# Optimization experiments

Hardware: AMD Instinct MI355X
Metric: run time of the kernel (lower is better)

Reference implementation:

```python
import jax, jax.numpy as jnp
import numpy as np
import math

B, C, BINS, W = 2, 8, 1024, 512
HEADS = 16
HD = BINS // HEADS          # 64 head dim
ROT = BINS // HEADS // 2    # 32 rotated dims
EXP = 4
EPS = 1e-5
MAX_FREQ = 10.0


def setup_inputs() -> dict:
    key = jax.random.key(0)
    ks = jax.random.split(key, 8)
    def u(k, shape, fan_in):
        lim = 1.0 / math.sqrt(fan_in)
        return jax.random.uniform(k, shape, jnp.float32, -lim, lim)
    return {
        "x": jax.random.normal(ks[0], (B, C, BINS, W), jnp.float32),
        "norm1_w": jnp.ones((BINS,), jnp.float32),
        "norm1_b": jnp.zeros((BINS,), jnp.float32),
        # 'pixel' rotary init: linspace(1, max_freq/2, dim//2) * pi (learned)
        "rot_freqs": jnp.linspace(1.0, MAX_FREQ / 2, ROT // 2, dtype=jnp.float32) * math.pi,
        "q_w": u(ks[1], (C, BINS, BINS), BINS),
        "out_w": u(ks[2], (C, BINS, BINS), BINS),
        "norm2_w": jnp.ones((BINS,), jnp.float32),
        "norm2_b": jnp.zeros((BINS,), jnp.float32),
        "lin1_w": u(ks[3], (C, BINS * EXP, BINS), BINS),
        "lin2_w": u(ks[4], (C, BINS, BINS * EXP), BINS * EXP),
    }


def _mlin(x, w):
    # x: [b,c,f_in,w]; w: [c,f_out,f_in] -> [b,c,f_out,w]
    return jnp.einsum('bcfw,cgf->bcgw', x, w)


def _frame_norm(x, w, b):
    # LayerNorm over the bins axis (axis=2) of [b,c,bins,w]
    m = jnp.mean(x, axis=2, keepdims=True)
    v = jnp.var(x, axis=2, keepdims=True)
    xn = (x - m) * jax.lax.rsqrt(v + EPS)
    return xn * w[:, None] + b[:, None]


def _rotate(q, cos, sin):
    # q: [b,c,h,w,d]; rotate first ROT dims with interleaved-pair rotate_half
    q1, q2 = q[..., :ROT], q[..., ROT:]
    qp = q1.reshape(*q1.shape[:-1], ROT // 2, 2)
    rh = jnp.stack([-qp[..., 1], qp[..., 0]], axis=-1).reshape(q1.shape)
    return jnp.concatenate([q1 * cos + rh * sin, q2], axis=-1)


def _attention(x, rot_freqs, q_w, out_w):
    b, c, bins, w = x.shape
    # faithful to source: q, k, v ALL use q_proj
    y = _mlin(x, q_w)  # [b,c,bins,w]
    # -> [b,c,h,w,d]
    y = y.transpose(0, 1, 3, 2).reshape(b, c, w, HEADS, HD).transpose(0, 1, 3, 2, 4)
    # rotary angles: t * freqs, repeat-interleaved x2 -> [w, ROT]
    t = jnp.arange(w, dtype=jnp.float32)
    ang = jnp.repeat(t[:, None] * rot_freqs[None, :], 2, axis=-1)
    cos, sin = jnp.cos(ang), jnp.sin(ang)
    q = _rotate(y, cos, sin)
    k = _rotate(y, cos, sin)
    v = y
    # NOTE: source scales by 1/sqrt(h) where h == bins (spectral height)
    scores = jnp.einsum('bchwd,bchud->bchwu', q, k) / math.sqrt(bins)
    a = jnp.einsum('bchwu,bchud->bchwd', jax.nn.softmax(scores, axis=-1), v)
    # [b,c,h,w,d] -> [b,c,bins,w]
    a = a.transpose(0, 1, 3, 2, 4).reshape(b, c, w, bins).transpose(0, 1, 3, 2)
    return _mlin(a, out_w)


def reference(x, norm1_w, norm1_b, rot_freqs, q_w, out_w,
              norm2_w, norm2_b, lin1_w, lin2_w):
    z = _frame_norm(x, norm1_w, norm1_b)
    z = _attention(z, rot_freqs, q_w, out_w)
    x = x + z  # dropout=0 -> identity
    z = _frame_norm(x, norm2_w, norm2_b)
    z = _mlin(jax.nn.gelu(_mlin(z, lin1_w), approximate=False), lin2_w)
    return x + z
```

## Files before the change

### kernel.cpp

```cpp
#include <hip/hip_runtime.h>
#include <math.h>

#define BB 2
#define CCH 8
#define BINS 1024
#define WW 512
#define HEADS 16
#define HD 64
#define ROTD 32
#define EXPF 4
#define NXE 8388608L
#define NTW 32

typedef unsigned short ushortT;
typedef short bf16x8 __attribute__((ext_vector_type(8)));
typedef float f32x4 __attribute__((ext_vector_type(4)));

__device__ __forceinline__ ushortT f2bf(float f) {
    unsigned int u = __float_as_uint(f);
    u = (u + 0x7FFF + ((u >> 16) & 1)) >> 16;
    return (ushortT)u;
}
__device__ __forceinline__ float bf2f(ushortT h) {
    return __uint_as_float(((unsigned int)h) << 16);
}
__device__ __forceinline__ unsigned int cvtpk(float lo, float hi) {
    unsigned int r;
    asm("v_cvt_pk_bf16_f32 %0, %1, %2" : "=v"(r) : "v"(lo), "v"(hi));
    return r;
}
__device__ __forceinline__ float geluf(float x) {
    return 0.5f * x * (1.f + erff(x * 0.70710678118654752f));
}
__device__ __forceinline__ void gl_lds16(const ushortT* g, ushortT* l) {
    __builtin_amdgcn_global_load_lds(
        (const __attribute__((address_space(1))) unsigned int*)g,
        (__attribute__((address_space(3))) unsigned int*)l, 16, 0, 0);
}
__device__ __forceinline__ void cast8(const float* s, ushortT* d) {
    float4 a = *(const float4*)s;
    float4 b = *(const float4*)(s + 4);
    uint4 v;
    v.x = cvtpk(a.x, a.y); v.y = cvtpk(a.z, a.w);
    v.z = cvtpk(b.x, b.y); v.w = cvtpk(b.z, b.w);
    *(uint4*)d = v;
}

__global__ __launch_bounds__(1024)
void normT_k(const float* __restrict__ X, const float* __restrict__ wgt,
             const float* __restrict__ bia, ushortT* __restrict__ YT)
{
    __shared__ float tile[NTW][BINS + 1];
    __shared__ float red0[32][NTW], red1[32][NTW];
    __shared__ float ms[NTW], is[NTW];
    const int bc = blockIdx.x >> 4;
    const int w0 = (blockIdx.x & 15) * NTW;
    const int tid = threadIdx.x;
    const int w  = tid & (NTW - 1);
    const int fy = tid >> 5;
    const float* Xb = X + (long)bc * BINS * WW + w0;
    float s = 0.f, s2 = 0.f;
    for (int f = fy; f < BINS; f += 32) {
        float v = Xb[(long)f * WW + w];
        s += v; s2 += v * v;
        tile[w][f] = v;
    }
    red0[fy][w] = s; red1[fy][w] = s2;
    __syncthreads();
    if (tid < NTW) {
        float ss = 0.f, qq = 0.f;
        #pragma unroll
        for (int j = 0; j < 32; ++j) { ss += red0[j][tid]; qq += red1[j][tid]; }
        float m = ss * (1.f / BINS);
        float var = qq * (1.f / BINS) - m * m;
        ms[tid] = m; is[tid] = rsqrtf(var + 1e-5f);
    }
    __syncthreads();
    const int w2 = tid >> 5;
    const int c  = tid & 31;
    float m = ms[w2], inv = is[w2];
    ushortT* Yb = YT + ((long)bc * WW + w0 + w2) * BINS;
    #pragma unroll
    for (int jj = 0; jj < 4; ++jj) {
        int f0 = jj * 256 + c * 8;
        union { ushortT h[8]; uint4 v; } r;
        #pragma unroll
        for (int e = 0; e < 8; ++e) {
            int f = f0 + e;
            float v = (tile[w2][f] - m) * inv * wgt[f] + bia[f];
            r.h[e] = f2bf(v);
        }
        *(uint4*)&Yb[f0] = r.v;
    }
}

__global__ void rope_tab_k(const float* __restrict__ freqs,
                           float* __restrict__ cosT, float* __restrict__ sinT)
{
    int idx = blockIdx.x * 256 + threadIdx.x;
    if (idx >= WW * 16) return;
    int w = idx >> 4, i = idx & 15;
    float ang = (float)w * freqs[i];
    cosT[idx] = cosf(ang);
    sinT[idx] = sinf(ang);
}

__global__ __launch_bounds__(256)
void mattn_k(const ushortT* __restrict__ rotT, const ushortT* __restrict__ yT,
             ushortT* __restrict__ oT,
             const float* __restrict__ wsrc, ushortT* __restrict__ wdst)
{
    __shared__ ushortT Qs[64 * 64];
    __shared__ ushortT Ks[64 * 64];
    __shared__ ushortT Vs[64 * 72];
    __shared__ ushortT Ps[64 * 72];
    const int z = blockIdx.y;
    const int bc = z >> 4, h = z & 15;
    const int wq0 = blockIdx.x * 64;
    const int tid = threadIdx.x;
    const int wv = tid >> 6, l = tid & 63;
    const int lr = l & 15, lk = l >> 4;
    const long hbase = (long)bc * WW * 1024 + h * 64;

    #pragma unroll
    for (int p = 0; p < 2; ++p) {
        int r0 = p * 32 + wv * 8;
        int row = r0 + (l >> 3);
        int gs = (l & 7) ^ (row & 7);
        gl_lds16(rotT + hbase + (long)(wq0 + row) * 1024 + gs * 8, Qs + r0 * 64);
    }

    f32x4 oacc[4] = {};
    float mrow[4] = {-INFINITY, -INFINITY, -INFINITY, -INFINITY};
    float lrow[4] = {0.f, 0.f, 0.f, 0.f};

    for (int u0 = 0; u0 < WW; u0 += 64) {
        #pragma unroll
        for (int p = 0; p < 2; ++p) {
            int r0 = p * 32 + wv * 8;
            int row = r0 + (l >> 3);
            int gs = (l & 7) ^ (row & 7);
            gl_lds16(rotT + hbase + (long)(u0 + row) * 1024 + gs * 8, Ks + r0 * 64);
        }
        #pragma unroll
        for (int rep = 0; rep < 2; ++rep) {
            int ch = rep * 4 + wv;
            union { uint4 v; ushortT h8[8]; } tmp;
            tmp.v = *(const uint4*)(yT + hbase + (long)(u0 + l) * 1024 + ch * 8);
            #pragma unroll
            for (int j = 0; j < 8; ++j)
                Vs[(ch * 8 + j) * 72 + l] = tmp.h8[j];
        }
        __syncthreads();

        f32x4 sacc[4] = {};
        #pragma unroll
        for (int ko = 0; ko < 2; ++ko) {
            int ar = wv * 16 + lr;
            bf16x8 aq = *(const bf16x8*)&Qs[ar * 64 + (((ko * 4) + lk) ^ (ar & 7)) * 8];
            #pragma unroll
            for (int f = 0; f < 4; ++f) {
                int br = f * 16 + lr;
                bf16x8 bk = *(const bf16x8*)&Ks[br * 64 + (((ko * 4) + lk) ^ (br & 7)) * 8];
                sacc[f] = __builtin_amdgcn_mfma_f32_16x16x32_bf16(aq, bk, sacc[f], 0, 0, 0);
            }
        }

        #pragma unroll
        for (int rg = 0; rg < 4; ++rg) {
            float s0 = sacc[0][rg] * (1.f / 32.f);
            float s1 = sacc[1][rg] * (1.f / 32.f);
            float s2 = sacc[2][rg] * (1.f / 32.f);
            float s3 = sacc[3][rg] * (1.f / 32.f);
            float mx = fmaxf(fmaxf(s0, s1), fmaxf(s2, s3));
            mx = fmaxf(mx, __shfl_xor(mx, 1));
            mx = fmaxf(mx, __shfl_xor(mx, 2));
            mx = fmaxf(mx, __shfl_xor(mx, 4));
            mx = fmaxf(mx, __shfl_xor(mx, 8));
            float mnew = fmaxf(mrow[rg], mx);
            float al = __expf(mrow[rg] - mnew);
            float p0 = __expf(s0 - mnew), p1 = __expf(s1 - mnew);
            float p2 = __expf(s2 - mnew), p3 = __expf(s3 - mnew);
            float rs = p0 + p1 + p2 + p3;
            rs += __shfl_xor(rs, 1);
            rs += __shfl_xor(rs, 2);
            rs += __shfl_xor(rs, 4);
            rs += __shfl_xor(rs, 8);
            lrow[rg] = lrow[rg] * al + rs;
            mrow[rg] = mnew;
            oacc[0][rg] *= al; oacc[1][rg] *= al;
            oacc[2][rg] *= al; oacc[3][rg] *= al;
            int prow = wv * 16 + lk * 4 + rg;
            Ps[prow * 72 +  0 + lr] = f2bf(p0);
            Ps[prow * 72 + 16 + lr] = f2bf(p1);
            Ps[prow * 72 + 32 + lr] = f2bf(p2);
            Ps[prow * 72 + 48 + lr] = f2bf(p3);
        }
        asm volatile("s_waitcnt lgkmcnt(0)" ::: "memory");

        #pragma unroll
        for (int ko = 0; ko < 2; ++ko) {
            int ar = wv * 16 + lr;
            bf16x8 ap = *(const bf16x8*)&Ps[ar * 72 + ko * 32 + lk * 8];
            #pragma unroll
            for (int f = 0; f < 4; ++f) {
                bf16x8 bv = *(const bf16x8*)&Vs[(f * 16 + lr) * 72 + ko * 32 + lk * 8];
                oacc[f] = __builtin_amdgcn_mfma_f32_16x16x32_bf16(ap, bv, oacc[f], 0, 0, 0);
            }
        }
        __syncthreads();
    }

    #pragma unroll
    for (int rg = 0; rg < 4; ++rg) {
        float inv = 1.f / lrow[rg];
        int w = wq0 + wv * 16 + lk * 4 + rg;
        long b2 = (long)bc * WW * 1024 + (long)w * 1024 + h * 64;
        #pragma unroll
        for (int f = 0; f < 4; ++f)
            oT[b2 + f * 16 + lr] = f2bf(oacc[f][rg] * inv);
    }

    if (wsrc) {
        long wbase = ((long)z * 8 + blockIdx.x) * 16384 + tid * 8;
        #pragma unroll
        for (int p = 0; p < 8; ++p) {
            long i = wbase + (long)p * 2048;
            cast8(wsrc + i, wdst + i);
        }
    }
}

#define QPHASE(QM, QN, STAGES, VMW)                                          \
  {                                                                          \
    bf16x8 a0_[4], a1_[4], b0_[2], b1_[2];                                   \
    _Pragma("unroll")                                                        \
    for (int i = 0; i < 4; ++i) {                                            \
        int ra = wr * 128 + QM * 64 + i * 16 + lrow;                         \
        a0_[i] = *(const bf16x8*)&As[ra * 64 + ((lk    ) ^ (ra & 7)) * 8];   \
        a1_[i] = *(const bf16x8*)&As[ra * 64 + ((lk + 4) ^ (ra & 7)) * 8];   \
    }                                                                        \
    _Pragma("unroll")                                                        \
    for (int j = 0; j < 2; ++j) {                                            \
        int rb = wc * 64 + QN * 32 + j * 16 + lrow;                          \
        b0_[j] = *(const bf16x8*)&Bs[rb * 64 + ((lk    ) ^ (rb & 7)) * 8];   \
        b1_[j] = *(const bf16x8*)&Bs[rb * 64 + ((lk + 4) ^ (rb & 7)) * 8];   \
    }                                                                        \
    STAGES;                                                                  \
    VMW;                                                                     \
    asm volatile("s_waitcnt lgkmcnt(0)" ::: "memory");                       \
    __builtin_amdgcn_s_barrier();                                            \
    __builtin_amdgcn_s_setprio(1);                                           \
    _Pragma("unroll")                                                        \
    for (int i = 0; i < 4; ++i)                                              \
        _Pragma("unroll")                                                    \
        for (int j = 0; j < 2; ++j)                                          \
            acc[QM * 4 + i][QN * 2 + j] =                                    \
                __builtin_amdgcn_mfma_f32_16x16x32_bf16(                     \
                    a0_[i], b0_[j], acc[QM * 4 + i][QN * 2 + j], 0, 0, 0);   \
    _Pragma("unroll")                                                        \
    for (int i = 0; i < 4; ++i)                                              \
        _Pragma("unroll")                                                    \
        for (int j = 0; j < 2; ++j)                                          \
            acc[QM * 4 + i][QN * 2 + j] =                                    \
                __builtin_amdgcn_mfma_f32_16x16x32_bf16(                     \
                    a1_[i], b1_[j], acc[QM * 4 + i][QN * 2 + j], 0, 0, 0);   \
    __builtin_amdgcn_s_setprio(0);                                           \
  }

template<bool HASRES, bool GELUF, bool TRANSOUT>
__global__ __launch_bounds__(512)
void gemm8_k(const ushortT* __restrict__ A, long sA, int aMod,
             const ushortT* __restrict__ B, long sB,
             void* __restrict__ Cp, long sC,
             const float* __restrict__ R, long sR,
             const float* __restrict__ wsrc, ushortT* __restrict__ wdst,
             int M, int N, int K, int gx, int gy)
{
    __shared__ ushortT smem[65536];
    const int nwg = gridDim.x;
    const int bid = blockIdx.x;
    const int lid = (bid & 7) * (nwg >> 3) + (bid >> 3);
    const int x = lid % gx;
    const int y = (lid / gx) % gy;
    const int z = lid / (gx * gy);
    const ushortT* Ab = A + (long)(z % aMod) * sA + (long)y * 256 * K;
    const ushortT* Bb = B + (long)z * sB + (long)x * 256 * K;
    const int tid = threadIdx.x;
    const int wv = tid >> 6, l = tid & 63;
    const int lrow = l & 15, lk = l >> 4;
    const int wr = wv >> 2, wc = wv & 3;
    f32x4 acc[8][4] = {};
    const int NT = K >> 6;

    auto stageAh = [&](int T, int qm) {
        ushortT* D = smem + (T & 1) * 32768;
        const int k0 = T << 6;
        #pragma unroll
        for (int t = 0; t < 2; ++t) {
            int r0 = wv * 16 + t * 8;
            int gr0 = ((r0 & 64) << 1) + qm * 64 + (r0 & 63);
            int gr = gr0 + (l >> 3);
            int gs = (l & 7) ^ (gr & 7);
            gl_lds16(Ab + (long)gr * K + k0 + gs * 8, D + gr0 * 64);
        }
    };
    auto stageBh = [&](int T, int qn) {
        ushortT* D = smem + (T & 1) * 32768 + 16384;
        const int k0 = T << 6;
        #pragma unroll
        for (int t = 0; t < 2; ++t) {
            int r0 = wv * 16 + t * 8;
            int gr0 = ((r0 >> 5) << 6) + qn * 32 + (r0 & 31);
            int gr = gr0 + (l >> 3);
            int gs = (l & 7) ^ (gr & 7);
            gl_lds16(Bb + (long)gr * K + k0 + gs * 8, D + gr0 * 64);
        }
    };

    stageAh(0, 0); stageAh(0, 1); stageBh(0, 0); stageBh(0, 1);
    if (NT > 1) {
        stageAh(1, 0); stageBh(1, 0);
        asm volatile("s_waitcnt vmcnt(4)" ::: "memory");
    } else {
        asm volatile("s_waitcnt vmcnt(0)" ::: "memory");
    }
    __builtin_amdgcn_s_barrier();

    for (int T = 0; T < NT; ++T) {
        const ushortT* As = smem + (T & 1) * 32768;
        const ushortT* Bs = As + 16384;
        const bool s1 = (T + 1 < NT), s2 = (T + 2 < NT);
        QPHASE(0, 0, if (s1) stageAh(T + 1, 1), );
        QPHASE(0, 1, if (s1) stageBh(T + 1, 1), );
        QPHASE(1, 0, if (s2) stageAh(T + 2, 0), );
        QPHASE(1, 1, if (s2) stageBh(T + 2, 0),
               if (s2) { asm volatile("s_waitcnt vmcnt(4)" ::: "memory"); }
               else    { asm volatile("s_waitcnt vmcnt(0)" ::: "memory"); });
    }

    const int m0g = y * 256 + wr * 128, n0g = x * 256 + wc * 64;
    if (!TRANSOUT) {
        float* Cf = (float*)Cp + (long)z * sC;
        #pragma unroll
        for (int ip = 0; ip < 8; ++ip)
            #pragma unroll
            for (int j = 0; j < 4; ++j)
                #pragma unroll
                for (int rg = 0; rg < 4; ++rg) {
                    long m = m0g + ip * 16 + lk * 4 + rg;
                    long n = n0g + j * 16 + lrow;
                    float v = acc[ip][j][rg];
                    if (GELUF) v = geluf(v);
                    if (HASRES) v += R[(long)z * sR + m * N + n];
                    Cf[m * N + n] = v;
                }
    } else {
        __syncthreads();
        ushortT* Ts = smem + wv * 4096;
        ushortT* CT = (ushortT*)Cp + (long)z * sC;
        #pragma unroll
        for (int s = 0; s < 2; ++s) {
            #pragma unroll
            for (int i2 = 0; i2 < 4; ++i2)
                #pragma unroll
                for (int j = 0; j < 4; ++j)
                    #pragma unroll
                    for (int rg = 0; rg < 4; ++rg) {
                        int ml = i2 * 16 + lk * 4 + rg;
                        int nl = j * 16 + lrow;
                        float v = acc[s * 4 + i2][j][rg];
                        if (GELUF) v = geluf(v);
                        Ts[nl * 64 + (((ml >> 3) ^ (nl & 7)) << 3) + (ml & 7)] = f2bf(v);
                    }
            #pragma unroll
            for (int p = 0; p < 8; ++p) {
                int nl = p * 8 + (l >> 3), mc = l & 7;
                uint4 d = *(const uint4*)&Ts[nl * 64 + ((mc ^ (nl & 7)) << 3)];
                *(uint4*)&CT[(long)(n0g + nl) * M + m0g + s * 64 + mc * 8] = d;
            }
        }
    }

    if (wsrc) {
        long wbase = (long)bid * 65536 + tid * 8;
        #pragma unroll
        for (int p = 0; p < 16; ++p) {
            long i = wbase + (long)p * 4096;
            cast8(wsrc + i, wdst + i);
        }
    }
}

template<bool HASRES, bool GELUF, bool TRANSOUT>
__global__ __launch_bounds__(512)
void pgemm_k(const ushortT* __restrict__ A, long sA, int aMod,
             const ushortT* __restrict__ B, long sB,
             void* __restrict__ Cp, long sC,
             const float* __restrict__ R, long sR,
             int M, int N, int K, int gx, int gy)
{
    __shared__ ushortT smem[3 * 24576];
    const int nwg = gridDim.x;
    const int bid = blockIdx.x;
    const int lid = (bid & 7) * (nwg >> 3) + (bid >> 3);
    const int x = lid % gx;
    const int y = (lid / gx) % gy;
    const int z = lid / (gx * gy);
    const ushortT* Ab = A + (long)(z % aMod) * sA + (long)y * 128 * K;
    const ushortT* Bb = B + (long)z * sB + (long)x * 256 * K;
    const int tid = threadIdx.x;
    const int wv = tid >> 6, l = tid & 63;
    const int lrow = l & 15, lk = l >> 4;
    const int mb = (wv >> 2) * 64;
    const int nb = (wv & 3) * 64;
    f32x4 acc[4][4] = {};
    const int NT = K >> 6;

    auto stageA = [&](int T) {
        ushortT* As = smem + (T % 3) * 24576;
        const int k0 = T << 6;
        #pragma unroll
        for (int t = 0; t < 2; ++t) {
            int r0 = wv * 16 + t * 8;
            int row = r0 + (l >> 3);
            int gs = (l & 7) ^ (row & 7);
            gl_lds16(Ab + (long)row * K + k0 + gs * 8, As + r0 * 64);
        }
    };
    auto stageBh = [&](int T, int h) {
        ushortT* Bs = smem + (T % 3) * 24576 + 8192;
        const int k0 = T << 6;
        #pragma unroll
        for (int t = 0; t < 2; ++t) {
            int r0 = wv * 32 + (h * 2 + t) * 8;
            int row = r0 + (l >> 3);
            int gs = (l & 7) ^ (row & 7);
            gl_lds16(Bb + (long)row * K + k0 + gs * 8, Bs + r0 * 64);
        }
    };

    stageA(0); stageBh(0, 0); stageBh(0, 1);
    if (NT > 1) {
        stageA(1); stageBh(1, 0); stageBh(1, 1);
        asm volatile("s_waitcnt vmcnt(6)" ::: "memory");
    } else {
        asm volatile("s_waitcnt vmcnt(0)" ::: "memory");
    }
    __builtin_amdgcn_s_barrier();

    for (int T = 0; T < NT; ++T) {
        const ushortT* As = smem + (T % 3) * 24576;
        const ushortT* Bs = As + 8192;
        const bool s1 = (T + 1 < NT), s2 = (T + 2 < NT);

        {
            bf16x8 af[4], bg[4];
            #pragma unroll
            for (int i = 0; i < 4; ++i) {
                int ra = mb + i * 16 + lrow;
                af[i] = *(const bf16x8*)&As[ra * 64 + ((lk) ^ (ra & 7)) * 8];
                int rb = nb + i * 16 + lrow;
                bg[i] = *(const bf16x8*)&Bs[rb * 64 + ((lk) ^ (rb & 7)) * 8];
            }
            if (s2) { stageA(T + 2); stageBh(T + 2, 0); }
            asm volatile("s_waitcnt lgkmcnt(0)" ::: "memory");
            __builtin_amdgcn_s_barrier();
            __builtin_amdgcn_s_setprio(1);
            #pragma unroll
            for (int i = 0; i < 4; ++i)
                #pragma unroll
                for (int j = 0; j < 4; ++j)
                    acc[i][j] = __builtin_amdgcn_mfma_f32_16x16x32_bf16(
                        af[i], bg[j], acc[i][j], 0, 0, 0);
            __builtin_amdgcn_s_setprio(0);
        }
        {
            bf16x8 af[4], bg[4];
            #pragma unroll
            for (int i = 0; i < 4; ++i) {
                int ra = mb + i * 16 + lrow;
                af[i] = *(const bf16x8*)&As[ra * 64 + ((lk + 4) ^ (ra & 7)) * 8];
                int rb = nb + i * 16 + lrow;
                bg[i] = *(const bf16x8*)&Bs[rb * 64 + ((lk + 4) ^ (rb & 7)) * 8];
            }
            if (s2) stageBh(T + 2, 1);
            if (s1) {
                if (s2) { asm volatile("s_waitcnt vmcnt(6)" ::: "memory"); }
                else    { asm volatile("s_waitcnt vmcnt(0)" ::: "memory"); }
            }
            asm volatile("s_waitcnt lgkmcnt(0)" ::: "memory");
            __builtin_amdgcn_s_barrier();
            __builtin_amdgcn_s_setprio(1);
            #pragma unroll
            for (int i = 0; i < 4; ++i)
                #pragma unroll
                for (int j = 0; j < 4; ++j)
                    acc[i][j] = __builtin_amdgcn_mfma_f32_16x16x32_bf16(
                        af[i], bg[j], acc[i][j], 0, 0, 0);
            __builtin_amdgcn_s_setprio(0);
        }
    }

    const int m0g = y * 128 + mb, n0g = x * 256 + nb;
    if (!TRANSOUT) {
        float* Cf = (float*)Cp + (long)z * sC;
        #pragma unroll
        for (int i = 0; i < 4; ++i)
            #pragma unroll
            for (int j = 0; j < 4; ++j)
                #pragma unroll
                for (int rg = 0; rg < 4; ++rg) {
                    long m = m0g + i * 16 + lk * 4 + rg;
                    long n = n0g + j * 16 + lrow;
                    float v = acc[i][j][rg];
                    if (GELUF) v = geluf(v);
                    if (HASRES) v += R[(long)z * sR + m * N + n];
                    Cf[m * N + n] = v;
                }
    } else {
        __syncthreads();
        ushortT* Ts = smem + wv * 4096;
        #pragma unroll
        for (int i = 0; i < 4; ++i)
            #pragma unroll
            for (int j = 0; j < 4; ++j)
                #pragma unroll
                for (int rg = 0; rg < 4; ++rg) {
                    int ml = i * 16 + lk * 4 + rg;
                    int nl = j * 16 + lrow;
                    float v = acc[i][j][rg];
                    if (GELUF) v = geluf(v);
                    Ts[nl * 64 + (((ml >> 3) ^ (nl & 7)) << 3) + (ml & 7)] = f2bf(v);
                }
        __syncthreads();
        ushortT* CT = (ushortT*)Cp + (long)z * sC;
        #pragma unroll
        for (int p = 0; p < 8; ++p) {
            int nl = p * 8 + (l >> 3), mc = l & 7;
            uint4 d = *(const uint4*)&Ts[nl * 64 + ((mc ^ (nl & 7)) << 3)];
            *(uint4*)&CT[(long)(n0g + nl) * M + m0g + mc * 8] = d;
        }
    }
}

template<bool HASRES, bool GELUF, bool TRANSOUT, bool ROPE>
__global__ __launch_bounds__(256)
void fgemm_k(const float* __restrict__ A, long sA, int aMod,
             const ushortT* __restrict__ B, long sB,
             void* __restrict__ Cp, long sC,
             const float* __restrict__ R, long sR,
             ushortT* __restrict__ Crot,
             const float* __restrict__ cosT, const float* __restrict__ sinT,
             int M, int N, int K, int gx, int gy)
{
    __shared__ ushortT smem[2 * 8192];
    ushortT* As = smem;
    ushortT* Bs = smem + 8192;
    const int nwg = gridDim.x;
    const int bid = blockIdx.x;
    const int lid = (bid & 7) * (nwg >> 3) + (bid >> 3);
    const int x = lid % gx;
    const int y = (lid / gx) % gy;
    const int z = lid / (gx * gy);
    const float*   Ab = A + (long)(z % aMod) * sA + (long)y * 128 * K;
    const ushortT* Bb = B + (long)z * sB + (long)x * 128 * K;
    const int tid = threadIdx.x;
    const int wv = tid >> 6, l = tid & 63;
    const int lrow = l & 15, lk = l >> 4;
    const int mb = (wv >> 1) * 64, nb = (wv & 1) * 64;
    const int arow = tid >> 3, agrp = tid & 7;
    f32x4 acc[4][4] = {};
    float4 a0[4], a1[4];
    const int NT = K >> 6;

    auto fetchA = [&](int k0) {
        #pragma unroll
        for (int c = 0; c < 4; ++c) {
            const float* src = Ab + (long)(arow + c * 32) * K + k0 + agrp * 8;
            a0[c] = *(const float4*)src;
            a1[c] = *(const float4*)(src + 4);
        }
    };
    auto commitA = [&]() {
        #pragma unroll
        for (int c = 0; c < 4; ++c) {
            int row = arow + c * 32;
            uint4 v;
            v.x = cvtpk(a0[c].x, a0[c].y);
            v.y = cvtpk(a0[c].z, a0[c].w);
            v.z = cvtpk(a1[c].x, a1[c].y);
            v.w = cvtpk(a1[c].z, a1[c].w);
            *(uint4*)&As[row * 64 + ((agrp ^ (row & 7)) << 3)] = v;
        }
    };
    auto stageB = [&](int k0) {
        #pragma unroll
        for (int t = 0; t < 4; ++t) {
            int r0 = wv * 32 + t * 8;
            int row = r0 + (l >> 3);
            int gs = (l & 7) ^ (row & 7);
            gl_lds16(Bb + (long)row * K + k0 + gs * 8, Bs + r0 * 64);
        }
    };
    auto compute = [&]() {
        #pragma unroll
        for (int ko = 0; ko < 2; ++ko) {
            bf16x8 af[4], bg[4];
            #pragma unroll
            for (int i = 0; i < 4; ++i) {
                int ra = mb + i * 16 + lrow;
                af[i] = *(const bf16x8*)&As[ra * 64 + ((lk + ko * 4) ^ (ra & 7)) * 8];
                int rb = nb + i * 16 + lrow;
                bg[i] = *(const bf16x8*)&Bs[rb * 64 + ((lk + ko * 4) ^ (rb & 7)) * 8];
            }
            #pragma unroll
            for (int i = 0; i < 4; ++i)
                #pragma unroll
                for (int j = 0; j < 4; ++j)
                    acc[i][j] = __builtin_amdgcn_mfma_f32_16x16x32_bf16(
                        af[i], bg[j], acc[i][j], 0, 0, 0);
        }
    };

    fetchA(0);
    for (int t = 0; t < NT; ++t) {
        if (t > 0) __syncthreads();
        stageB(t << 6);
        commitA();
        if (t + 1 < NT) fetchA((t + 1) << 6);
        __syncthreads();
        compute();
    }

    const int m0g = y * 128 + mb, n0g = x * 128 + nb;
    if (!TRANSOUT) {
        float* Cf = (float*)Cp + (long)z * sC;
        #pragma unroll
        for (int i = 0; i < 4; ++i)
            #pragma unroll
            for (int j = 0; j < 4; ++j)
                #pragma unroll
                for (int rg = 0; rg < 4; ++rg) {
                    long m = m0g + i * 16 + lk * 4 + rg;
                    long n = n0g + j * 16 + lrow;
                    float v = acc[i][j][rg];
                    if (GELUF) v = geluf(v);
                    if (HASRES) v += R[(long)z * sR + m * N + n];
                    Cf[m * N + n] = v;
                }
    } else {
        ushortT* Ts = smem + wv * 4096;
        __syncthreads();
        #pragma unroll
        for (int i = 0; i < 4; ++i)
            #pragma unroll
            for (int j = 0; j < 4; ++j)
                #pragma unroll
                for (int rg = 0; rg < 4; ++rg) {
                    int ml = i * 16 + lk * 4 + rg;
                    int nl = j * 16 + lrow;
                    float v = acc[i][j][rg];
                    if (GELUF) v = geluf(v);
                    Ts[nl * 64 + (((ml >> 3) ^ (nl & 7)) << 3) + (ml & 7)] = f2bf(v);
                }
        __syncthreads();
        ushortT* CT = (ushortT*)Cp + (long)z * sC;
        #pragma unroll
        for (int p = 0; p < 8; ++p) {
            int nl = p * 8 + (l >> 3), mc = l & 7;
            uint4 d = *(const uint4*)&Ts[nl * 64 + ((mc ^ (nl & 7)) << 3)];
            int wg = n0g + nl;
            int g0 = m0g + mc * 8;
            *(uint4*)&CT[(long)wg * M + g0] = d;
            if (ROPE) {
                ushortT* RT = Crot + (long)z * sC;
                int d0 = g0 & 63;
                if (d0 >= ROTD) {
                    *(uint4*)&RT[(long)wg * M + g0] = d;
                } else {
                    union { uint4 v; ushortT h8[8]; } in, ov;
                    in.v = d;
                    #pragma unroll
                    for (int j = 0; j < 8; j += 2) {
                        int i2 = (d0 + j) >> 1;
                        float cc = cosT[wg * 16 + i2], ss = sinT[wg * 16 + i2];
                        float a = bf2f(in.h8[j]), b = bf2f(in.h8[j + 1]);
                        ov.h8[j]     = f2bf(a * cc - b * ss);
                        ov.h8[j + 1] = f2bf(b * cc + a * ss);
                    }
                    *(uint4*)&RT[(long)wg * M + g0] = ov.v;
                }
            }
        }
    }
}

extern "C" void kernel_launch(void* const* d_in, const int* in_sizes, int n_in,
                              void* d_out, int out_size, void* d_ws, size_t ws_size,
                              hipStream_t stream)
{
    const float* x    = (const float*)d_in[0];
    const float* n1w  = (const float*)d_in[1];
    const float* n1b  = (const float*)d_in[2];
    const float* freqs= (const float*)d_in[3];
    const float* qw   = (const float*)d_in[4];
    const float* ow   = (const float*)d_in[5];
    const float* n2w  = (const float*)d_in[6];
    const float* n2b  = (const float*)d_in[7];
    const float* l1w  = (const float*)d_in[8];
    const float* l2w  = (const float*)d_in[9];
    float* out = (float*)d_out;
    char* wsb  = (char*)d_ws;
    const long MB = 1L << 20;

    ushortT* znT  = (ushortT*)(wsb +   0 * MB);
    ushortT* yT   = (ushortT*)(wsb +  16 * MB);
    ushortT* rotT = (ushortT*)(wsb +  32 * MB);
    ushortT* CfT  = (ushortT*)(wsb +  48 * MB);
    ushortT* zn2T = (ushortT*)(wsb +  64 * MB);
    ushortT* h1T  = (ushortT*)(wsb +  80 * MB);
    ushortT* wB1  = (ushortT*)(wsb + 144 * MB);
    ushortT* wB2  = (ushortT*)(wsb +   0 * MB);
    float*   cosT = (float*)  (wsb + 208 * MB);
    float*   sinT = cosT + WW * 16;

    rope_tab_k<<<32, 256, 0, stream>>>(freqs, cosT, sinT);

    normT_k<<<BB * CCH * 16, 1024, 0, stream>>>(x, n1w, n1b, znT);

    fgemm_k<false, false, true, true><<<512, 256, 0, stream>>>(
        qw,  (long)BINS * BINS, CCH,
        znT, (long)WW * BINS,
        yT,  (long)WW * BINS,
        nullptr, 0,
        rotT, cosT, sinT,
        BINS, WW, BINS, 4, 8);

    mattn_k<<<dim3(8, 256), 256, 0, stream>>>(rotT, yT, CfT, l1w, wB1);

    fgemm_k<true, false, false, false><<<512, 256, 0, stream>>>(
        ow,  (long)BINS * BINS, CCH,
        CfT, (long)WW * BINS,
        out, (long)BINS * WW,
        x,   (long)BINS * WW,
        nullptr, nullptr, nullptr,
        BINS, WW, BINS, 4, 8);

    normT_k<<<BB * CCH * 16, 1024, 0, stream>>>(out, n2w, n2b, zn2T);

    gemm8_k<false, true, true><<<512, 512, 0, stream>>>(
        wB1,  (long)BINS * EXPF * BINS, CCH,
        zn2T, (long)WW * BINS,
        h1T,  (long)WW * BINS * EXPF,
        nullptr, 0,
        l2w, wB2,
        BINS * EXPF, WW, BINS, 2, 16);

    pgemm_k<true, false, false><<<256, 512, 0, stream>>>(
        wB2, (long)BINS * BINS * EXPF, CCH,
        h1T, (long)WW * BINS * EXPF,
        out, (long)BINS * WW,
        out, (long)BINS * WW,
        BINS, WW, BINS * EXPF, 2, 8);
}
```

Before: 426.5 us.

## Move weight fp32-to-bf16 casts into dedicated producer warps overlapping compute

Adds an extra wavefront to the attention and lin1 GEMM kernels that converts the next stage's fp32 weights to bf16 while the other waves compute. It replaces the tail-end cast loops that ran serially after the main work. Block-wide __syncthreads are swapped for raw s_barrier calls, and the extra wave issues matching barrier counts so every wave stays in step. The cost is a larger block and fragile barrier-count matching between the cast wave and the compute waves.

```diff
diff --git a/kernel.cpp b/kernel.cpp
--- a/kernel.cpp
+++ b/kernel.cpp
@@ -36,14 +36,6 @@
     __builtin_amdgcn_global_load_lds(
         (const __attribute__((address_space(1))) unsigned int*)g,
         (__attribute__((address_space(3))) unsigned int*)l, 16, 0, 0);
-}
-__device__ __forceinline__ void cast8(const float* s, ushortT* d) {
-    float4 a = *(const float4*)s;
-    float4 b = *(const float4*)(s + 4);
-    uint4 v;
-    v.x = cvtpk(a.x, a.y); v.y = cvtpk(a.z, a.w);
-    v.z = cvtpk(b.x, b.y); v.w = cvtpk(b.z, b.w);
-    *(uint4*)d = v;
 }
 
 __global__ __launch_bounds__(1024)
@@ -105,7 +97,7 @@
     sinT[idx] = sinf(ang);
 }
 
-__global__ __launch_bounds__(256)
+__global__ __launch_bounds__(320)
 void mattn_k(const ushortT* __restrict__ rotT, const ushortT* __restrict__ yT,
              ushortT* __restrict__ oT,
              const float* __restrict__ wsrc, ushortT* __restrict__ wdst)
@@ -122,6 +114,35 @@
     const int lr = l & 15, lk = l >> 4;
     const long hbase = (long)bc * WW * 1024 + h * 64;
 
+    if (wv == 4) {
+        const long bidl = (long)z * 8 + blockIdx.x;
+        const float* src = wsrc + bidl * 16384 + l * 8;
+        ushortT*     dst = wdst + bidl * 16384 + l * 8;
+        float4 q[4][2];
+        auto ld = [&](int c, int p) {
+            const float* sp = src + (long)c * 512;
+            q[p][0] = *(const float4*)sp;
+            q[p][1] = *(const float4*)(sp + 4);
+        };
+        auto st = [&](int c, int p) {
+            uint4 v;
+            v.x = cvtpk(q[p][0].x, q[p][0].y); v.y = cvtpk(q[p][0].z, q[p][0].w);
+            v.z = cvtpk(q[p][1].x, q[p][1].y); v.w = cvtpk(q[p][1].z, q[p][1].w);
+            *(uint4*)(dst + (long)c * 512) = v;
+        };
+        ld(0, 0); ld(1, 1); ld(2, 2); ld(3, 3);
+        #pragma unroll
+        for (int s = 0; s < 8; ++s) {
+            st(s * 4 + 0, 0); st(s * 4 + 1, 1);
+            if (s * 4 + 4 < 32) { ld(s * 4 + 4, 0); ld(s * 4 + 5, 1); }
+            __builtin_amdgcn_s_barrier();
+            st(s * 4 + 2, 2); st(s * 4 + 3, 3);
+            if (s * 4 + 6 < 32) { ld(s * 4 + 6, 2); ld(s * 4 + 7, 3); }
+            __builtin_amdgcn_s_barrier();
+        }
+        return;
+    }
+
     #pragma unroll
     for (int p = 0; p < 2; ++p) {
         int r0 = p * 32 + wv * 8;
@@ -151,7 +172,8 @@
             for (int j = 0; j < 8; ++j)
                 Vs[(ch * 8 + j) * 72 + l] = tmp.h8[j];
         }
-        __syncthreads();
+        asm volatile("s_waitcnt vmcnt(0) lgkmcnt(0)" ::: "memory");
+        __builtin_amdgcn_s_barrier();
 
         f32x4 sacc[4] = {};
         #pragma unroll
@@ -208,7 +230,7 @@
                 oacc[f] = __builtin_amdgcn_mfma_f32_16x16x32_bf16(ap, bv, oacc[f], 0, 0, 0);
             }
         }
-        __syncthreads();
+        __builtin_amdgcn_s_barrier();
     }
 
     #pragma unroll
@@ -219,15 +241,6 @@
         #pragma unroll
         for (int f = 0; f < 4; ++f)
             oT[b2 + f * 16 + lr] = f2bf(oacc[f][rg] * inv);
-    }
-
-    if (wsrc) {
-        long wbase = ((long)z * 8 + blockIdx.x) * 16384 + tid * 8;
-        #pragma unroll
-        for (int p = 0; p < 8; ++p) {
-            long i = wbase + (long)p * 2048;
-            cast8(wsrc + i, wdst + i);
-        }
     }
 }
 
@@ -269,7 +282,7 @@
   }
 
 template<bool HASRES, bool GELUF, bool TRANSOUT>
-__global__ __launch_bounds__(512)
+__global__ __launch_bounds__(576)
 void gemm8_k(const ushortT* __restrict__ A, long sA, int aMod,
              const ushortT* __restrict__ B, long sB,
              void* __restrict__ Cp, long sC,
@@ -290,8 +303,48 @@
     const int wv = tid >> 6, l = tid & 63;
     const int lrow = l & 15, lk = l >> 4;
     const int wr = wv >> 2, wc = wv & 3;
+    const int NT = K >> 6;
+
+    if (wv == 8) {
+        const float* src = wsrc + (long)bid * 65536 + l * 8;
+        ushortT*     dst = wdst + (long)bid * 65536 + l * 8;
+        float4 q[4][2];
+        auto ld = [&](int c, int p) {
+            const float* sp = src + (long)c * 512;
+            q[p][0] = *(const float4*)sp;
+            q[p][1] = *(const float4*)(sp + 4);
+        };
+        auto st = [&](int c, int p) {
+            uint4 v;
+            v.x = cvtpk(q[p][0].x, q[p][0].y); v.y = cvtpk(q[p][0].z, q[p][0].w);
+            v.z = cvtpk(q[p][1].x, q[p][1].y); v.w = cvtpk(q[p][1].z, q[p][1].w);
+            *(uint4*)(dst + (long)c * 512) = v;
+        };
+        ld(0, 0); ld(1, 1); ld(2, 2); ld(3, 3);
+        __builtin_amdgcn_s_barrier();
+        for (int s = 0; s < NT; ++s) {
+            int c0 = s * 8;
+            st(c0 + 0, 0); st(c0 + 1, 1);
+            if (c0 + 4 < 128) { ld(c0 + 4, 0); ld(c0 + 5, 1); }
+            __builtin_amdgcn_s_barrier();
+            st(c0 + 2, 2); st(c0 + 3, 3);
+            if (c0 + 6 < 128) { ld(c0 + 6, 2); ld(c0 + 7, 3); }
+            __builtin_amdgcn_s_barrier();
+            st(c0 + 4, 0); st(c0 + 5, 1);
+            if (c0 + 8 < 128) { ld(c0 + 8, 0); ld(c0 + 9, 1); }
+            __builtin_amdgcn_s_barrier();
+            st(c0 + 6, 2); st(c0 + 7, 3);
+            if (c0 + 10 < 128) { ld(c0 + 10, 2); ld(c0 + 11, 3); }
+            __builtin_amdgcn_s_barrier();
+        }
+        if (TRANSOUT) {
+            __builtin_amdgcn_s_barrier();
+            __builtin_amdgcn_s_barrier();
+        }
+        return;
+    }
+
     f32x4 acc[8][4] = {};
-    const int NT = K >> 6;
 
     auto stageAh = [&](int T, int qm) {
         ushortT* D = smem + (T & 1) * 32768;
@@ -356,11 +409,12 @@
                     Cf[m * N + n] = v;
                 }
     } else {
-        __syncthreads();
+        __builtin_amdgcn_s_barrier();
         ushortT* Ts = smem + wv * 4096;
         ushortT* CT = (ushortT*)Cp + (long)z * sC;
         #pragma unroll
         for (int s = 0; s < 2; ++s) {
+            if (s == 1) { asm volatile("s_waitcnt lgkmcnt(0)" ::: "memory"); }
             #pragma unroll
             for (int i2 = 0; i2 < 4; ++i2)
                 #pragma unroll
@@ -373,21 +427,14 @@
                         if (GELUF) v = geluf(v);
                         Ts[nl * 64 + (((ml >> 3) ^ (nl & 7)) << 3) + (ml & 7)] = f2bf(v);
                     }
+            if (s == 0) { __builtin_amdgcn_s_barrier(); }
+            asm volatile("s_waitcnt lgkmcnt(0)" ::: "memory");
             #pragma unroll
             for (int p = 0; p < 8; ++p) {
                 int nl = p * 8 + (l >> 3), mc = l & 7;
                 uint4 d = *(const uint4*)&Ts[nl * 64 + ((mc ^ (nl & 7)) << 3)];
                 *(uint4*)&CT[(long)(n0g + nl) * M + m0g + s * 64 + mc * 8] = d;
             }
-        }
-    }
-
-    if (wsrc) {
-        long wbase = (long)bid * 65536 + tid * 8;
-        #pragma unroll
-        for (int p = 0; p < 16; ++p) {
-            long i = wbase + (long)p * 4096;
-            cast8(wsrc + i, wdst + i);
         }
     }
 }
@@ -737,7 +784,7 @@
         rotT, cosT, sinT,
         BINS, WW, BINS, 4, 8);
 
-    mattn_k<<<dim3(8, 256), 256, 0, stream>>>(rotT, yT, CfT, l1w, wB1);
+    mattn_k<<<dim3(8, 256), 320, 0, stream>>>(rotT, yT, CfT, l1w, wB1);
 
     fgemm_k<true, false, false, false><<<512, 256, 0, stream>>>(
         ow,  (long)BINS * BINS, CCH,
@@ -749,7 +796,7 @@
 
     normT_k<<<BB * CCH * 16, 1024, 0, stream>>>(out, n2w, n2b, zn2T);
 
-    gemm8_k<false, true, true><<<512, 512, 0, stream>>>(
+    gemm8_k<false, true, true><<<512, 576, 0, stream>>>(
         wB1,  (long)BINS * EXPF * BINS, CCH,
         zn2T, (long)WW * BINS,
         h1T,  (long)WW * BINS * EXPF,
```

Result: slower. 782.6 us (+83.5%).

## Move weight casts into extra GEMM blocks instead of kernel tails

Applied to the files above, without the earlier changes.

The fp32-to-bf16 weight casts for lin1 and lin2 were appended to the tail of every attention and GEMM block. They now run in dedicated extra workgroups added to the Q-projection GEMM and the lin1 GEMM grids. The extra workgroups cast in parallel with the compute blocks rather than lengthening each block's critical path. Tile swizzling now uses the compute-block count, and extra barriers were added around the transposed epilogue's shared-memory staging, which costs some sync overhead.

```diff
diff --git a/kernel.cpp b/kernel.cpp
--- a/kernel.cpp
+++ b/kernel.cpp
@@ -107,8 +107,7 @@
 
 __global__ __launch_bounds__(256)
 void mattn_k(const ushortT* __restrict__ rotT, const ushortT* __restrict__ yT,
-             ushortT* __restrict__ oT,
-             const float* __restrict__ wsrc, ushortT* __restrict__ wdst)
+             ushortT* __restrict__ oT)
 {
     __shared__ ushortT Qs[64 * 64];
     __shared__ ushortT Ks[64 * 64];
@@ -219,15 +218,6 @@
         #pragma unroll
         for (int f = 0; f < 4; ++f)
             oT[b2 + f * 16 + lr] = f2bf(oacc[f][rg] * inv);
-    }
-
-    if (wsrc) {
-        long wbase = ((long)z * 8 + blockIdx.x) * 16384 + tid * 8;
-        #pragma unroll
-        for (int p = 0; p < 8; ++p) {
-            long i = wbase + (long)p * 2048;
-            cast8(wsrc + i, wdst + i);
-        }
     }
 }
 
@@ -275,18 +265,28 @@
              void* __restrict__ Cp, long sC,
              const float* __restrict__ R, long sR,
              const float* __restrict__ wsrc, ushortT* __restrict__ wdst,
-             int M, int N, int K, int gx, int gy)
+             int ncomp, int M, int N, int K, int gx, int gy)
 {
     __shared__ ushortT smem[65536];
-    const int nwg = gridDim.x;
     const int bid = blockIdx.x;
-    const int lid = (bid & 7) * (nwg >> 3) + (bid >> 3);
+    const int tid = threadIdx.x;
+
+    if (bid >= ncomp) {
+        const long base = (long)(bid - ncomp) * 131072;
+        #pragma unroll 4
+        for (int c = 0; c < 32; ++c) {
+            long i = base + (long)c * 4096 + tid * 8;
+            cast8(wsrc + i, wdst + i);
+        }
+        return;
+    }
+
+    const int lid = (bid & 7) * (ncomp >> 3) + (bid >> 3);
     const int x = lid % gx;
     const int y = (lid / gx) % gy;
     const int z = lid / (gx * gy);
     const ushortT* Ab = A + (long)(z % aMod) * sA + (long)y * 256 * K;
     const ushortT* Bb = B + (long)z * sB + (long)x * 256 * K;
-    const int tid = threadIdx.x;
     const int wv = tid >> 6, l = tid & 63;
     const int lrow = l & 15, lk = l >> 4;
     const int wr = wv >> 2, wc = wv & 3;
@@ -373,21 +373,14 @@
                         if (GELUF) v = geluf(v);
                         Ts[nl * 64 + (((ml >> 3) ^ (nl & 7)) << 3) + (ml & 7)] = f2bf(v);
                     }
+            __syncthreads();
             #pragma unroll
             for (int p = 0; p < 8; ++p) {
                 int nl = p * 8 + (l >> 3), mc = l & 7;
                 uint4 d = *(const uint4*)&Ts[nl * 64 + ((mc ^ (nl & 7)) << 3)];
                 *(uint4*)&CT[(long)(n0g + nl) * M + m0g + s * 64 + mc * 8] = d;
             }
-        }
-    }
-
-    if (wsrc) {
-        long wbase = (long)bid * 65536 + tid * 8;
-        #pragma unroll
-        for (int p = 0; p < 16; ++p) {
-            long i = wbase + (long)p * 4096;
-            cast8(wsrc + i, wdst + i);
+            __syncthreads();
         }
     }
 }
@@ -552,20 +545,31 @@
              const float* __restrict__ R, long sR,
              ushortT* __restrict__ Crot,
              const float* __restrict__ cosT, const float* __restrict__ sinT,
-             int M, int N, int K, int gx, int gy)
+             const float* __restrict__ wsrc, ushortT* __restrict__ wdst,
+             int ncomp, int M, int N, int K, int gx, int gy)
 {
     __shared__ ushortT smem[2 * 8192];
     ushortT* As = smem;
     ushortT* Bs = smem + 8192;
-    const int nwg = gridDim.x;
     const int bid = blockIdx.x;
-    const int lid = (bid & 7) * (nwg >> 3) + (bid >> 3);
+    const int tid = threadIdx.x;
+
+    if (bid >= ncomp) {
+        const long base = (long)(bid - ncomp) * 131072;
+        #pragma unroll 4
+        for (int c = 0; c < 64; ++c) {
+            long i = base + (long)c * 2048 + tid * 8;
+            cast8(wsrc + i, wdst + i);
+        }
+        return;
+    }
+
+    const int lid = (bid & 7) * (ncomp >> 3) + (bid >> 3);
     const int x = lid % gx;
     const int y = (lid / gx) % gy;
     const int z = lid / (gx * gy);
     const float*   Ab = A + (long)(z % aMod) * sA + (long)y * 128 * K;
     const ushortT* Bb = B + (long)z * sB + (long)x * 128 * K;
-    const int tid = threadIdx.x;
     const int wv = tid >> 6, l = tid & 63;
     const int lrow = l & 15, lk = l >> 4;
     const int mb = (wv >> 1) * 64, nb = (wv & 1) * 64;
@@ -729,15 +733,16 @@
 
     normT_k<<<BB * CCH * 16, 1024, 0, stream>>>(x, n1w, n1b, znT);
 
-    fgemm_k<false, false, true, true><<<512, 256, 0, stream>>>(
+    fgemm_k<false, false, true, true><<<768, 256, 0, stream>>>(
         qw,  (long)BINS * BINS, CCH,
         znT, (long)WW * BINS,
         yT,  (long)WW * BINS,
         nullptr, 0,
         rotT, cosT, sinT,
-        BINS, WW, BINS, 4, 8);
-
-    mattn_k<<<dim3(8, 256), 256, 0, stream>>>(rotT, yT, CfT, l1w, wB1);
+        l1w, wB1,
+        512, BINS, WW, BINS, 4, 8);
+
+    mattn_k<<<dim3(8, 256), 256, 0, stream>>>(rotT, yT, CfT);
 
     fgemm_k<true, false, false, false><<<512, 256, 0, stream>>>(
         ow,  (long)BINS * BINS, CCH,
@@ -745,17 +750,18 @@
         out, (long)BINS * WW,
         x,   (long)BINS * WW,
         nullptr, nullptr, nullptr,
-        BINS, WW, BINS, 4, 8);
+        nullptr, nullptr,
+        512, BINS, WW, BINS, 4, 8);
 
     normT_k<<<BB * CCH * 16, 1024, 0, stream>>>(out, n2w, n2b, zn2T);
 
-    gemm8_k<false, true, true><<<512, 512, 0, stream>>>(
+    gemm8_k<false, true, true><<<768, 512, 0, stream>>>(
         wB1,  (long)BINS * EXPF * BINS, CCH,
         zn2T, (long)WW * BINS,
         h1T,  (long)WW * BINS * EXPF,
         nullptr, 0,
         l2w, wB2,
-        BINS * EXPF, WW, BINS, 2, 16);
+        512, BINS * EXPF, WW, BINS, 2, 16);
 
     pgemm_k<true, false, false><<<256, 512, 0, stream>>>(
         wB2, (long)BINS * BINS * EXPF, CCH,
```

New measurement: 437.7 us. 1.03x slower.
